# Performance work log

Hardware: AMD Instinct MI355X
Metric: run time of the kernel (lower is better)

Reference implementation:

```python
import jax, jax.numpy as jnp
import numpy as np

B, T, C, H = 4, 2048, 1024, 16
D = C // H  # head_dim = 64
SCALE = D ** -0.5


def setup_inputs() -> dict:
    key = jax.random.key(0)
    ks = jax.random.split(key, 5)
    s = C ** -0.5
    return {
        "x": jax.random.normal(ks[0], (B, T, C), dtype=jnp.float32),
        "W_qkv": jax.random.normal(ks[1], (C, 3 * C), dtype=jnp.float32) * s,
        "b_qkv": jnp.zeros((3 * C,), dtype=jnp.float32),
        "W_out": jax.random.normal(ks[2], (C, C), dtype=jnp.float32) * s,
        "b_out": jnp.zeros((C,), dtype=jnp.float32),
    }


def reference(x, W_qkv, b_qkv, W_out, b_out):
    Bx, Tx, Cx = x.shape
    qkv = x @ W_qkv + b_qkv                      # [B,T,3C]
    qkv = qkv.reshape(Bx, Tx, 3, H, D)
    q, k, v = qkv[:, :, 0], qkv[:, :, 1], qkv[:, :, 2]  # [B,T,H,D]
    # scores [B,H,T,T]
    scores = jnp.einsum("bthd,bshd->bhts", q, k) * SCALE
    causal = jnp.tril(jnp.ones((Tx, Tx), dtype=bool))
    scores = jnp.where(causal[None, None], scores, -jnp.inf)
    probs = jax.nn.softmax(scores, axis=-1)
    out = jnp.einsum("bhts,bshd->bthd", probs, v).reshape(Bx, Tx, Cx)
    return out @ W_out + b_out
```

## Files before the change

kernel.cpp:

```cpp
#include <hip/hip_runtime.h>
#include <cstdint>
#include <cstddef>

#define B_ 4
#define T_ 2048
#define C_ 1024
#define H_ 16
#define D_ 64
#define SCALE_ 0.125f

typedef _Float16 f16;
typedef f16 f16x4 __attribute__((ext_vector_type(4)));
typedef f16 f16x8 __attribute__((ext_vector_type(8)));
typedef float f32x4 __attribute__((ext_vector_type(4)));

__device__ __forceinline__ void async_ld16(const void* g, void* l) {
  __builtin_amdgcn_global_load_lds(
      (const __attribute__((address_space(1))) void*)g,
      (__attribute__((address_space(3))) void*)l,
      16, 0, 0);
}

__global__ void k_cvt(const float* __restrict__ in, f16* __restrict__ out, int n4) {
  int i = blockIdx.x * 256 + threadIdx.x;
  if (i >= n4) return;
  float4 v = ((const float4*)in)[i];
  f16x4 h;
  h.x = (f16)v.x; h.y = (f16)v.y; h.z = (f16)v.z; h.w = (f16)v.w;
  ((f16x4*)out)[i] = h;
}

__global__ void k_tconv(const float* __restrict__ in, f16* __restrict__ out, int K, int N) {
  __shared__ float tile[32][33];
  int tx = threadIdx.x & 31, ty = threadIdx.x >> 5;
  int k0 = blockIdx.y * 32, n0 = blockIdx.x * 32;
#pragma unroll
  for (int i = 0; i < 32; i += 8)
    tile[ty + i][tx] = in[(size_t)(k0 + ty + i) * N + n0 + tx];
  __syncthreads();
#pragma unroll
  for (int i = 0; i < 32; i += 8)
    out[(size_t)(n0 + ty + i) * K + k0 + tx] = (f16)tile[tx][ty + i];
}

__global__ void k_vtrans(const f16* __restrict__ QKV, f16* __restrict__ Vt) {
  __shared__ f16 tile[32][33];
  int tx = threadIdx.x & 31, ty = threadIdx.x >> 5;
  int t0 = blockIdx.x * 32, d0 = blockIdx.y * 32;
  int bh = blockIdx.z, b = bh >> 4, h = bh & 15;
#pragma unroll
  for (int i = 0; i < 32; i += 8)
    tile[ty + i][tx] = QKV[(size_t)(b * T_ + t0 + ty + i) * (3 * C_) + 2 * C_ + h * D_ + d0 + tx];
  __syncthreads();
#pragma unroll
  for (int i = 0; i < 32; i += 8)
    Vt[((size_t)bh * D_ + d0 + ty + i) * T_ + t0 + tx] = tile[tx][ty + i];
}

__global__ __launch_bounds__(256, 2)
void k_gemm_bt(const f16* __restrict__ A, const f16* __restrict__ Bt,
               const float* __restrict__ bias, f16* __restrict__ Ch,
               float* __restrict__ Cf, int M, int N, int K)
{
  __shared__ __align__(16) f16 As[128 * 32];
  __shared__ __align__(16) f16 Bs[128 * 32];
  const int t = threadIdx.x;
  const int wave = t >> 6, lane = t & 63, lr = lane & 15, quad = lane >> 4;
  const int bn = blockIdx.x, bm = blockIdx.y;
  const int row0 = bm * 128, col0 = bn * 128;
  const int wm = (wave >> 1) * 64, wn = (wave & 1) * 64;

  f32x4 acc[4][4] = {};

  const f16* gA = A + (size_t)(row0 + (t >> 2)) * K + (t & 3) * 8;
  const f16* gB = Bt + (size_t)(col0 + (t >> 2)) * K + (t & 3) * 8;
  const size_t rowskip = (size_t)64 * K;
  f16* lA = As + wave * 512;
  f16* lB = Bs + wave * 512;

  for (int k0 = 0; k0 < K; k0 += 32) {
    async_ld16(gA + k0,           lA);
    async_ld16(gA + rowskip + k0, lA + 2048);
    async_ld16(gB + k0,           lB);
    async_ld16(gB + rowskip + k0, lB + 2048);
    __syncthreads();

    f16x8 af[4], bf[4];
#pragma unroll
    for (int i = 0; i < 4; ++i) {
      af[i] = *(const f16x8*)&As[(wm + i * 16 + lr) * 32 + quad * 8];
      bf[i] = *(const f16x8*)&Bs[(wn + i * 16 + lr) * 32 + quad * 8];
    }
#pragma unroll
    for (int mi = 0; mi < 4; ++mi)
#pragma unroll
      for (int ni = 0; ni < 4; ++ni)
        acc[mi][ni] = __builtin_amdgcn_mfma_f32_16x16x32_f16(af[mi], bf[ni], acc[mi][ni], 0, 0, 0);
    __syncthreads();
  }

#pragma unroll
  for (int mi = 0; mi < 4; ++mi) {
#pragma unroll
    for (int ni = 0; ni < 4; ++ni) {
      int col = col0 + wn + ni * 16 + lr;
      float bv = bias[col];
#pragma unroll
      for (int r = 0; r < 4; ++r) {
        int row = row0 + wm + mi * 16 + quad * 4 + r;
        float v = acc[mi][ni][r] + bv;
        if (Ch) Ch[(size_t)row * N + col] = (f16)v;
        else    Cf[(size_t)row * N + col] = v;
      }
    }
  }
}

__global__ __launch_bounds__(256, 4)
void k_flash(const f16* __restrict__ QKV, const f16* __restrict__ Vt, f16* __restrict__ O)
{
  __shared__ __align__(16) f16 Ks[2][64 * 64];
  __shared__ __align__(16) f16 Vs[2][64 * 64];
  __shared__ __align__(16) f16 Ps[4][16 * 64];

  const int a = blockIdx.x, bh = blockIdx.y;
  const int b = bh >> 4, h = bh & 15;
  const int qtA = a, qtB = 31 - a;
  const int t = threadIdx.x, wave = t >> 6, lane = t & 63, lr = lane & 15, quad = lane >> 4;
  const int lr3 = lr & 7;
  const int c0 = quad ^ lr3;
  const int c1 = c0 ^ 4;

  const f16 scl = (f16)0.125f;
  const f16* qpA = QKV + (size_t)(b * T_ + qtA * 64 + wave * 16 + lr) * 3072 + h * 64;
  const f16* qpB = QKV + (size_t)(b * T_ + qtB * 64 + wave * 16 + lr) * 3072 + h * 64;
  f16x8 qA0 = *(const f16x8*)(qpA + quad * 8)      * scl;
  f16x8 qA1 = *(const f16x8*)(qpA + 32 + quad * 8) * scl;
  f16x8 qB0 = *(const f16x8*)(qpB + quad * 8)      * scl;
  f16x8 qB1 = *(const f16x8*)(qpB + 32 + quad * 8) * scl;

  float lA_[4] = {0.f, 0.f, 0.f, 0.f};
  float lB_[4] = {0.f, 0.f, 0.f, 0.f};
  f32x4 oA[4] = {}, oB[4] = {};

  const int sw = ((t & 7) ^ ((t >> 3) & 7)) * 8;
  const f16* gK = QKV + (size_t)(b * T_ + (t >> 3)) * 3072 + 1024 + h * 64 + sw;
  const f16* gV = Vt + ((size_t)bh * 64 + (t >> 3)) * T_ + sw;

  f16* myP = Ps[wave];
  f16* pw0 = myP + (quad * 4) * 64 + ((0 ^ quad) << 4) + lr;
  f16* pw1 = myP + (quad * 4) * 64 + ((1 ^ quad) << 4) + lr;
  f16* pw2 = myP + (quad * 4) * 64 + ((2 ^ quad) << 4) + lr;
  f16* pw3 = myP + (quad * 4) * 64 + ((3 ^ quad) << 4) + lr;
  const f16* pr0 = myP + lr * 64 + ((((quad >> 1))     ^ (lr >> 2)) << 4) + ((quad & 1) << 3);
  const f16* pr1 = myP + lr * 64 + ((((quad >> 1) ^ 2) ^ (lr >> 2)) << 4) + ((quad & 1) << 3);

  const int last = qtB;

  {
    f16* lK = Ks[0] + wave * 512;
    f16* lV = Vs[0] + wave * 512;
    async_ld16(gK,                     lK);
    async_ld16(gK + (size_t)32 * 3072, lK + 2048);
    async_ld16(gV,                     lV);
    async_ld16(gV + (size_t)32 * T_,   lV + 2048);
  }

  for (int kt = 0; kt <= last; ++kt) {
    __syncthreads();
    const int buf = kt & 1;
    if (kt < last) {
      const f16* gk = gK + (size_t)((kt + 1) * 64) * 3072;
      const f16* gv = gV + (kt + 1) * 64;
      f16* lK = Ks[buf ^ 1] + wave * 512;
      f16* lV = Vs[buf ^ 1] + wave * 512;
      async_ld16(gk,                     lK);
      async_ld16(gk + (size_t)32 * 3072, lK + 2048);
      async_ld16(gv,                     lV);
      async_ld16(gv + (size_t)32 * T_,   lV + 2048);
    }
    const f16* K_ = Ks[buf];
    const f16* V_ = Vs[buf];
    const bool actA = (kt <= qtA);

    {
      f32x4 s4[4];
#pragma unroll
      for (int ni = 0; ni < 4; ++ni) {
        const f16* kr = K_ + (ni * 16 + lr) * 64;
        f16x8 k0 = *(const f16x8*)(kr + c0 * 8);
        f16x8 k1 = *(const f16x8*)(kr + c1 * 8);
        f32x4 z = {};
        z = __builtin_amdgcn_mfma_f32_16x16x32_f16(qB0, k0, z, 0, 0, 0);
        z = __builtin_amdgcn_mfma_f32_16x16x32_f16(qB1, k1, z, 0, 0, 0);
        s4[ni] = z;
      }
      if (kt == qtB) {
        const int rloc = wave * 16 + quad * 4;
#pragma unroll
        for (int r = 0; r < 4; ++r) {
#pragma unroll
          for (int ni = 0; ni < 4; ++ni)
            if (ni * 16 + lr > rloc + r) s4[ni][r] = -1e30f;
        }
      }
#pragma unroll
      for (int r = 0; r < 4; ++r) {
        float e0 = __expf(s4[0][r]), e1 = __expf(s4[1][r]);
        float e2 = __expf(s4[2][r]), e3 = __expf(s4[3][r]);
        lB_[r] += (e0 + e1) + (e2 + e3);
        pw0[r * 64] = (f16)e0; pw1[r * 64] = (f16)e1;
        pw2[r * 64] = (f16)e2; pw3[r * 64] = (f16)e3;
      }
      f16x8 pB0 = *(const f16x8*)pr0;
      f16x8 pB1 = *(const f16x8*)pr1;
#pragma unroll
      for (int ni = 0; ni < 4; ++ni) {
        const f16* vr = V_ + (ni * 16 + lr) * 64;
        f16x8 v0 = *(const f16x8*)(vr + c0 * 8);
        f16x8 v1 = *(const f16x8*)(vr + c1 * 8);
        oB[ni] = __builtin_amdgcn_mfma_f32_16x16x32_f16(pB0, v0, oB[ni], 0, 0, 0);
        oB[ni] = __builtin_amdgcn_mfma_f32_16x16x32_f16(pB1, v1, oB[ni], 0, 0, 0);
      }
    }

    if (actA) {
      f32x4 s4[4];
#pragma unroll
      for (int ni = 0; ni < 4; ++ni) {
        const f16* kr = K_ + (ni * 16 + lr) * 64;
        f16x8 k0 = *(const f16x8*)(kr + c0 * 8);
        f16x8 k1 = *(const f16x8*)(kr + c1 * 8);
        f32x4 z = {};
        z = __builtin_amdgcn_mfma_f32_16x16x32_f16(qA0, k0, z, 0, 0, 0);
        z = __builtin_amdgcn_mfma_f32_16x16x32_f16(qA1, k1, z, 0, 0, 0);
        s4[ni] = z;
      }
      if (kt == qtA) {
        const int rloc = wave * 16 + quad * 4;
#pragma unroll
        for (int r = 0; r < 4; ++r) {
#pragma unroll
          for (int ni = 0; ni < 4; ++ni)
            if (ni * 16 + lr > rloc + r) s4[ni][r] = -1e30f;
        }
      }
#pragma unroll
      for (int r = 0; r < 4; ++r) {
        float e0 = __expf(s4[0][r]), e1 = __expf(s4[1][r]);
        float e2 = __expf(s4[2][r]), e3 = __expf(s4[3][r]);
        lA_[r] += (e0 + e1) + (e2 + e3);
        pw0[r * 64] = (f16)e0; pw1[r * 64] = (f16)e1;
        pw2[r * 64] = (f16)e2; pw3[r * 64] = (f16)e3;
      }
      f16x8 pA0 = *(const f16x8*)pr0;
      f16x8 pA1 = *(const f16x8*)pr1;
#pragma unroll
      for (int ni = 0; ni < 4; ++ni) {
        const f16* vr = V_ + (ni * 16 + lr) * 64;
        f16x8 v0 = *(const f16x8*)(vr + c0 * 8);
        f16x8 v1 = *(const f16x8*)(vr + c1 * 8);
        oA[ni] = __builtin_amdgcn_mfma_f32_16x16x32_f16(pA0, v0, oA[ni], 0, 0, 0);
        oA[ni] = __builtin_amdgcn_mfma_f32_16x16x32_f16(pA1, v1, oA[ni], 0, 0, 0);
      }
    }
  }

#pragma unroll
  for (int r = 0; r < 4; ++r) {
    float la = lA_[r], lb = lB_[r];
#pragma unroll
    for (int off = 1; off < 16; off <<= 1) {
      la += __shfl_xor(la, off, 64);
      lb += __shfl_xor(lb, off, 64);
    }
    const int rowA = qtA * 64 + wave * 16 + quad * 4 + r;
    const int rowB = qtB * 64 + wave * 16 + quad * 4 + r;
    float invA = 1.f / la;
    float invB = 1.f / lb;
#pragma unroll
    for (int ni = 0; ni < 4; ++ni) {
      O[(size_t)(b * T_ + rowA) * C_ + h * 64 + ni * 16 + lr] = (f16)(oA[ni][r] * invA);
      O[(size_t)(b * T_ + rowB) * C_ + h * 64 + ni * 16 + lr] = (f16)(oB[ni][r] * invB);
    }
  }
}

extern "C" void kernel_launch(void* const* d_in, const int* in_sizes, int n_in,
                              void* d_out, int out_size, void* d_ws, size_t ws_size,
                              hipStream_t stream)
{
  const float* x    = (const float*)d_in[0];
  const float* Wqkv = (const float*)d_in[1];
  const float* bqkv = (const float*)d_in[2];
  const float* Wout = (const float*)d_in[3];
  const float* bout = (const float*)d_in[4];
  float* out = (float*)d_out;

  f16* xh    = (f16*)d_ws;
  f16* WqkvT = xh + (size_t)8192 * 1024;
  f16* WoutT = WqkvT + (size_t)3072 * 1024;
  f16* QKV   = WoutT + (size_t)1024 * 1024;
  f16* VtG   = QKV + (size_t)8192 * 3072;
  f16* Oh    = VtG + (size_t)64 * 64 * 2048;

  k_cvt<<<8192, 256, 0, stream>>>(x, xh, 8192 * 1024 / 4);
  k_tconv<<<dim3(3072 / 32, 1024 / 32), 256, 0, stream>>>(Wqkv, WqkvT, 1024, 3072);
  k_tconv<<<dim3(1024 / 32, 1024 / 32), 256, 0, stream>>>(Wout, WoutT, 1024, 1024);

  k_gemm_bt<<<dim3(3072 / 128, 8192 / 128), 256, 0, stream>>>(
      xh, WqkvT, bqkv, QKV, nullptr, 8192, 3072, 1024);

  k_vtrans<<<dim3(T_ / 32, D_ / 32, B_ * H_), 256, 0, stream>>>(QKV, VtG);

  k_flash<<<dim3(16, B_ * H_), 256, 0, stream>>>(QKV, VtG, Oh);

  k_gemm_bt<<<dim3(1024 / 128, 8192 / 128), 256, 0, stream>>>(
      Oh, WoutT, bout, nullptr, out, 8192, 1024, 1024);
}
```

Before: 276.6 us.

## Double-buffer GEMM LDS tiles with XOR swizzle and fuse prep kernels

The projection GEMM now keeps two LDS buffers, issuing the async global-to-LDS loads for the next k-slice before computing the current one. This drops one barrier per iteration and overlaps load latency with MFMA work. LDS columns are XOR-swizzled to cut bank conflicts on the fragment reads, and launch bounds move to three blocks per CU. The three conversion/transpose kernels are merged into one launch to save launch overhead. In exchange each block uses twice the LDS, which may limit how many blocks fit per CU, and the higher occupancy target could cause register spills.

```diff
diff --git a/kernel.cpp b/kernel.cpp
--- a/kernel.cpp
+++ b/kernel.cpp
@@ -21,19 +21,30 @@
       16, 0, 0);
 }
 
-__global__ void k_cvt(const float* __restrict__ in, f16* __restrict__ out, int n4) {
-  int i = blockIdx.x * 256 + threadIdx.x;
-  if (i >= n4) return;
-  float4 v = ((const float4*)in)[i];
-  f16x4 h;
-  h.x = (f16)v.x; h.y = (f16)v.y; h.z = (f16)v.z; h.w = (f16)v.w;
-  ((f16x4*)out)[i] = h;
-}
-
-__global__ void k_tconv(const float* __restrict__ in, f16* __restrict__ out, int K, int N) {
+__global__ void k_prep(const float* __restrict__ x, f16* __restrict__ xh,
+                       const float* __restrict__ Wqkv, f16* __restrict__ WqkvT,
+                       const float* __restrict__ Wout, f16* __restrict__ WoutT)
+{
   __shared__ float tile[32][33];
-  int tx = threadIdx.x & 31, ty = threadIdx.x >> 5;
-  int k0 = blockIdx.y * 32, n0 = blockIdx.x * 32;
+  const int bx = blockIdx.x, t = threadIdx.x;
+  if (bx < 8192) {
+    int i = bx * 256 + t;
+    float4 v = ((const float4*)x)[i];
+    f16x4 h;
+    h.x = (f16)v.x; h.y = (f16)v.y; h.z = (f16)v.z; h.w = (f16)v.w;
+    ((f16x4*)xh)[i] = h;
+    return;
+  }
+  const float* in; f16* out; int K, N, nt, kt;
+  if (bx < 8192 + 3072) {
+    int idx = bx - 8192; in = Wqkv; out = WqkvT; K = 1024; N = 3072;
+    nt = idx % 96; kt = idx / 96;
+  } else {
+    int idx = bx - 11264; in = Wout; out = WoutT; K = 1024; N = 1024;
+    nt = idx % 32; kt = idx / 32;
+  }
+  int tx = t & 31, ty = t >> 5;
+  int k0 = kt * 32, n0 = nt * 32;
 #pragma unroll
   for (int i = 0; i < 32; i += 8)
     tile[ty + i][tx] = in[(size_t)(k0 + ty + i) * N + n0 + tx];
@@ -57,46 +68,62 @@
     Vt[((size_t)bh * D_ + d0 + ty + i) * T_ + t0 + tx] = tile[tx][ty + i];
 }
 
-__global__ __launch_bounds__(256, 2)
+__global__ __launch_bounds__(256, 3)
 void k_gemm_bt(const f16* __restrict__ A, const f16* __restrict__ Bt,
                const float* __restrict__ bias, f16* __restrict__ Ch,
                float* __restrict__ Cf, int M, int N, int K)
 {
-  __shared__ __align__(16) f16 As[128 * 32];
-  __shared__ __align__(16) f16 Bs[128 * 32];
+  __shared__ __align__(16) f16 As[2][128 * 32];
+  __shared__ __align__(16) f16 Bs[2][128 * 32];
   const int t = threadIdx.x;
   const int wave = t >> 6, lane = t & 63, lr = lane & 15, quad = lane >> 4;
-  const int bn = blockIdx.x, bm = blockIdx.y;
-  const int row0 = bm * 128, col0 = bn * 128;
+  const int row0 = blockIdx.y * 128, col0 = blockIdx.x * 128;
   const int wm = (wave >> 1) * 64, wn = (wave & 1) * 64;
 
   f32x4 acc[4][4] = {};
 
-  const f16* gA = A + (size_t)(row0 + (t >> 2)) * K + (t & 3) * 8;
-  const f16* gB = Bt + (size_t)(col0 + (t >> 2)) * K + (t & 3) * 8;
+  const int sw = ((t & 3) ^ ((t >> 4) & 3)) * 8;
+  const f16* gA = A + (size_t)(row0 + (t >> 2)) * K + sw;
+  const f16* gB = Bt + (size_t)(col0 + (t >> 2)) * K + sw;
   const size_t rowskip = (size_t)64 * K;
-  f16* lA = As + wave * 512;
-  f16* lB = Bs + wave * 512;
-
-  for (int k0 = 0; k0 < K; k0 += 32) {
-    async_ld16(gA + k0,           lA);
-    async_ld16(gA + rowskip + k0, lA + 2048);
-    async_ld16(gB + k0,           lB);
-    async_ld16(gB + rowskip + k0, lB + 2048);
+  const int rc = (quad ^ (lr >> 2)) * 8;
+
+  {
+    f16* lA = As[0] + wave * 512;
+    f16* lB = Bs[0] + wave * 512;
+    async_ld16(gA,           lA);
+    async_ld16(gA + rowskip, lA + 2048);
+    async_ld16(gB,           lB);
+    async_ld16(gB + rowskip, lB + 2048);
+  }
+
+  const int iters = K >> 5;
+  for (int it = 0; it < iters; ++it) {
     __syncthreads();
+    const int buf = it & 1;
+    if (it + 1 < iters) {
+      const int k0 = (it + 1) * 32;
+      f16* lA = As[buf ^ 1] + wave * 512;
+      f16* lB = Bs[buf ^ 1] + wave * 512;
+      async_ld16(gA + k0,           lA);
+      async_ld16(gA + rowskip + k0, lA + 2048);
+      async_ld16(gB + k0,           lB);
+      async_ld16(gB + rowskip + k0, lB + 2048);
+    }
+    const f16* As_ = As[buf];
+    const f16* Bs_ = Bs[buf];
 
     f16x8 af[4], bf[4];
 #pragma unroll
     for (int i = 0; i < 4; ++i) {
-      af[i] = *(const f16x8*)&As[(wm + i * 16 + lr) * 32 + quad * 8];
-      bf[i] = *(const f16x8*)&Bs[(wn + i * 16 + lr) * 32 + quad * 8];
+      af[i] = *(const f16x8*)&As_[(wm + i * 16 + lr) * 32 + rc];
+      bf[i] = *(const f16x8*)&Bs_[(wn + i * 16 + lr) * 32 + rc];
     }
 #pragma unroll
     for (int mi = 0; mi < 4; ++mi)
 #pragma unroll
       for (int ni = 0; ni < 4; ++ni)
         acc[mi][ni] = __builtin_amdgcn_mfma_f32_16x16x32_f16(af[mi], bf[ni], acc[mi][ni], 0, 0, 0);
-    __syncthreads();
   }
 
 #pragma unroll
@@ -304,9 +331,7 @@
   f16* VtG   = QKV + (size_t)8192 * 3072;
   f16* Oh    = VtG + (size_t)64 * 64 * 2048;
 
-  k_cvt<<<8192, 256, 0, stream>>>(x, xh, 8192 * 1024 / 4);
-  k_tconv<<<dim3(3072 / 32, 1024 / 32), 256, 0, stream>>>(Wqkv, WqkvT, 1024, 3072);
-  k_tconv<<<dim3(1024 / 32, 1024 / 32), 256, 0, stream>>>(Wout, WoutT, 1024, 1024);
+  k_prep<<<12288, 256, 0, stream>>>(x, xh, Wqkv, WqkvT, Wout, WoutT);
 
   k_gemm_bt<<<dim3(3072 / 128, 8192 / 128), 256, 0, stream>>>(
       xh, WqkvT, bqkv, QKV, nullptr, 8192, 3072, 1024);
```

Result: no change. 274.3 us (-0.8%).
